# Optimization experiments

Measured on AMD Instinct MI355X. Metric: run time of the kernel, lower is better.

The kernel has to match this reference:

```python
import jax, jax.numpy as jnp
import numpy as np

N = 50000
IN_F = 200
OUT_F = 200
NRELA = 200
E1 = 400000
E2 = 100000
ALPHA = 0.2  # leakyrelu slope


def setup_inputs() -> dict:
    key = jax.random.key(0)
    ks = jax.random.split(key, 9)
    xav = float(np.sqrt(2.0 / (OUT_F + 2 * IN_F + NRELA))) * 1.414
    return {
        "x": jax.random.normal(ks[0], (N, IN_F), dtype=jnp.float32),
        "edge": jax.random.randint(ks[1], (2, E1), 0, N, dtype=jnp.int32),
        "edge_embed": jax.random.normal(ks[2], (E1, NRELA), dtype=jnp.float32),
        "edge_list_nhop": jax.random.randint(ks[3], (2, E2), 0, N, dtype=jnp.int32),
        "edge_embed_nhop": jax.random.normal(ks[4], (E2, NRELA), dtype=jnp.float32),
        "a": jax.random.normal(ks[5], (OUT_F, 2 * IN_F + NRELA), dtype=jnp.float32) * xav,
        "a_2": jax.random.normal(ks[6], (1, OUT_F), dtype=jnp.float32) * float(np.sqrt(2.0 / (1 + OUT_F))) * 1.414,
        "mlp_w": jax.random.normal(ks[7], (1, OUT_F), dtype=jnp.float32) * float(np.sqrt(1.0 / OUT_F)),
        "mlp_b": jnp.zeros((1,), dtype=jnp.float32),
    }


def reference(x, edge, edge_embed, edge_list_nhop, edge_embed_nhop, a, a_2, mlp_w, mlp_b):
    # concat 1-hop and n-hop edges: e [2,E], emb [E,nrela]
    e = jnp.concatenate([edge, edge_list_nhop], axis=1)
    emb = jnp.concatenate([edge_embed, edge_embed_nhop], axis=0)
    src = e[0]
    dst = e[1]
    n_edges = emb.shape[0]
    # edge_h: [E, 2*in + nrela]
    edge_h = jnp.concatenate([x[src], x[dst], emb], axis=1)
    # edge_m = a @ edge_h.T, kept as [E, out]
    edge_m = edge_h @ a.T
    # powers = -leakyrelu(a_2 @ edge_m): [E]
    powers = -jax.nn.leaky_relu(edge_m @ a_2[0], ALPHA)
    # inline MLP: tanh(Linear(edge_m)) -> [E]
    y = jnp.tanh(edge_m @ mlp_w[0] + mlp_b[0])
    powers = powers * y / n_edges
    edge_e = jnp.exp(powers)  # [E]
    n = x.shape[0]
    # segment-sum over source nodes (sparse.sum over dim=1 of coo[src,dst,:])
    e_rowsum = jax.ops.segment_sum(edge_e, src, num_segments=n)[:, None]  # [N,1]
    e_rowsum = jnp.where(e_rowsum == 0.0, 1e-12, e_rowsum)
    # weighted scatter-add of edge messages
    edge_w = edge_e[:, None] * edge_m  # [E, out]
    h_prime = jax.ops.segment_sum(edge_w, src, num_segments=n)  # [N, out]
    h_prime = h_prime / e_rowsum
    return jax.nn.elu(h_prime)  # concat=True
```

## Files before the change

kernel.cpp:

```cpp
#include <hip/hip_runtime.h>
#include <math.h>

#define NN    50000
#define FDIM  200
#define E1N   400000
#define E2N   100000
#define EN    500000

typedef __attribute__((ext_vector_type(8))) short short8;
typedef __attribute__((ext_vector_type(4))) float f32x4;

#define VALL_OFF   0
#define WALL_OFF   608
#define SCAL_OFF   1216
#define RS_OFF     201216
#define CNT_OFF    251216
#define FILL_OFF   301216
#define INCL_OFF   351216
#define BSUM_OFF   401216
#define SORT_OFF   401472
#define XB_OFF     1401472
#define AB_OFF     6401472
#define TSB_OFF    6461472

static __device__ __forceinline__ unsigned short f2bf(float f) {
    unsigned int u = __float_as_uint(f);
    unsigned int r = (u + 0x7fffu + ((u >> 16) & 1u)) >> 16;
    return (unsigned short)r;
}
static __device__ __forceinline__ float bf2f(unsigned short s) {
    return __uint_as_float((unsigned int)s << 16);
}

__global__ void k_coeffs(const float* __restrict__ a, const float* __restrict__ a2,
                         const float* __restrict__ mlpw,
                         float* __restrict__ vall, float* __restrict__ wall) {
    int k = blockIdx.x * blockDim.x + threadIdx.x;
    if (k >= 600) return;
    float v = 0.f, w = 0.f;
    for (int o = 0; o < FDIM; ++o) {
        float av = a[o * 600 + k];
        v += a2[o] * av;
        w += mlpw[o] * av;
    }
    vall[k] = v;
    wall[k] = w;
}

__global__ __launch_bounds__(256) void k_node_scal(const float* __restrict__ x,
                                                   const float* __restrict__ vall,
                                                   const float* __restrict__ wall,
                                                   float* __restrict__ scal,
                                                   unsigned short* __restrict__ xb) {
    __shared__ float sv[1200];
    int tid = threadIdx.x;
    for (int i = tid; i < 1200; i += 256) sv[i] = (i < 600) ? vall[i] : wall[i - 600];
    __syncthreads();
    int lane = tid & 63;
    int n = blockIdx.x * 4 + (tid >> 6);
    float ps = 0.f, pd = 0.f, qs = 0.f, qd = 0.f;
    if (lane < 50) {
        float4 xv = *(const float4*)(x + (size_t)n * FDIM + lane * 4);
        float4 v1 = *(const float4*)(sv + lane * 4);
        float4 v2 = *(const float4*)(sv + 200 + lane * 4);
        float4 w1 = *(const float4*)(sv + 600 + lane * 4);
        float4 w2 = *(const float4*)(sv + 800 + lane * 4);
        ps = xv.x * v1.x + xv.y * v1.y + xv.z * v1.z + xv.w * v1.w;
        pd = xv.x * v2.x + xv.y * v2.y + xv.z * v2.z + xv.w * v2.w;
        qs = xv.x * w1.x + xv.y * w1.y + xv.z * w1.z + xv.w * w1.w;
        qd = xv.x * w2.x + xv.y * w2.y + xv.z * w2.z + xv.w * w2.w;
        ushort4 o;
        o.x = f2bf(xv.x); o.y = f2bf(xv.y); o.z = f2bf(xv.z); o.w = f2bf(xv.w);
        *(ushort4*)(xb + (size_t)n * FDIM + lane * 4) = o;
    }
    #pragma unroll
    for (int off = 32; off > 0; off >>= 1) {
        ps += __shfl_xor(ps, off);
        pd += __shfl_xor(pd, off);
        qs += __shfl_xor(qs, off);
        qd += __shfl_xor(qd, off);
    }
    if (lane == 0) {
        float4 r = make_float4(ps, pd, qs, qd);
        *(float4*)(scal + (size_t)n * 4) = r;
    }
}

__global__ __launch_bounds__(256) void k_cvt(const float* __restrict__ src,
                                             unsigned short* __restrict__ dst, int n4) {
    int i = blockIdx.x * 256 + threadIdx.x;
    if (i >= n4) return;
    float4 v = *(const float4*)(src + (size_t)i * 4);
    ushort4 o;
    o.x = f2bf(v.x); o.y = f2bf(v.y); o.z = f2bf(v.z); o.w = f2bf(v.w);
    *(ushort4*)(dst + (size_t)i * 4) = o;
}

__global__ __launch_bounds__(256) void k_hist(const int* __restrict__ edge,
                                              const int* __restrict__ edgenh,
                                              int* __restrict__ counts) {
    int g = blockIdx.x * 256 + threadIdx.x;
    if (g >= EN) return;
    int s = (g < E1N) ? edge[g] : edgenh[g - E1N];
    atomicAdd(counts + s, 1);
}

__global__ __launch_bounds__(256) void k_scan1(const int* __restrict__ counts,
                                               int* __restrict__ incl,
                                               int* __restrict__ bsums) {
    __shared__ int tmp[256];
    int g = blockIdx.x * 256 + threadIdx.x;
    int v = (g < NN) ? counts[g] : 0;
    tmp[threadIdx.x] = v;
    __syncthreads();
    for (int off = 1; off < 256; off <<= 1) {
        int t = (threadIdx.x >= off) ? tmp[threadIdx.x - off] : 0;
        __syncthreads();
        tmp[threadIdx.x] += t;
        __syncthreads();
    }
    if (g < NN) incl[g] = tmp[threadIdx.x];
    if (threadIdx.x == 255) bsums[blockIdx.x] = tmp[255];
}

__global__ __launch_bounds__(256) void k_scan2(int* __restrict__ bsums, int nb) {
    __shared__ int tmp[256];
    int v = (threadIdx.x < nb) ? bsums[threadIdx.x] : 0;
    tmp[threadIdx.x] = v;
    __syncthreads();
    for (int off = 1; off < 256; off <<= 1) {
        int t = (threadIdx.x >= off) ? tmp[threadIdx.x - off] : 0;
        __syncthreads();
        tmp[threadIdx.x] += t;
        __syncthreads();
    }
    if (threadIdx.x < nb) bsums[threadIdx.x] = tmp[threadIdx.x] - v;
}

__global__ __launch_bounds__(256) void k_scan3(const int* __restrict__ counts,
                                               int* __restrict__ incl,
                                               const int* __restrict__ bsums,
                                               int* __restrict__ fill) {
    int g = blockIdx.x * 256 + threadIdx.x;
    if (g >= NN) return;
    int v = incl[g] - counts[g] + bsums[blockIdx.x];
    incl[g] = v;
    fill[g] = v;
}

__global__ __launch_bounds__(256) void k_scatter(const int* __restrict__ edge,
                                                 const int* __restrict__ edgenh,
                                                 int* __restrict__ fill,
                                                 int2* __restrict__ sorted2) {
    int g = blockIdx.x * 256 + threadIdx.x;
    if (g >= EN) return;
    int s, d;
    if (g < E1N) { s = edge[g]; d = edge[E1N + g]; }
    else { s = edgenh[g - E1N]; d = edgenh[E2N + (g - E1N)]; }
    int pos = atomicAdd(fill + s, 1);
    sorted2[pos] = make_int2(g, d);
}

__global__ __launch_bounds__(256) void k_csr(const int2* __restrict__ sorted2,
                                             const int* __restrict__ offs,
                                             const int* __restrict__ counts,
                                             const float* __restrict__ ee,
                                             const float* __restrict__ eenh,
                                             const unsigned short* __restrict__ xb,
                                             const float* __restrict__ vall,
                                             const float* __restrict__ wall,
                                             const float* __restrict__ scal,
                                             const float* __restrict__ mlpb,
                                             float* __restrict__ rowsum,
                                             unsigned short* __restrict__ Tsb) {
    int tid = threadIdx.x, lane = tid & 63;
    int n = blockIdx.x * 4 + (tid >> 6);
    float4 v3 = make_float4(0, 0, 0, 0), w3 = v3;
    if (lane < 50) {
        v3 = *(const float4*)(vall + 400 + lane * 4);
        w3 = *(const float4*)(wall + 400 + lane * 4);
    }
    float4 sc_n = *(const float4*)(scal + (size_t)n * 4);
    float mb = mlpb[0];
    int beg = offs[n], cnt = counts[n];
    float accx0 = 0, accx1 = 0, accx2 = 0, accx3 = 0;
    float acce0 = 0, acce1 = 0, acce2 = 0, acce3 = 0;
    float rs = 0.f;
    int2 ed = (cnt > 0) ? sorted2[beg] : make_int2(0, 0);
    for (int i = 0; i < cnt; ++i) {
        int2 ed_n = (i + 1 < cnt) ? sorted2[beg + i + 1] : ed;
        int e = ed.x, d = ed.y;
        const float* erow = (e < E1N) ? ee + (size_t)e * FDIM
                                      : eenh + (size_t)(e - E1N) * FDIM;
        float4 ev = make_float4(0, 0, 0, 0), xv = ev;
        if (lane < 50) {
            ev = *(const float4*)(erow + lane * 4);
            ushort4 xu = *(const ushort4*)(xb + (size_t)d * FDIM + lane * 4);
            xv.x = bf2f(xu.x); xv.y = bf2f(xu.y); xv.z = bf2f(xu.z); xv.w = bf2f(xu.w);
        }
        float pe = ev.x * v3.x + ev.y * v3.y + ev.z * v3.z + ev.w * v3.w;
        float qe = ev.x * w3.x + ev.y * w3.y + ev.z * w3.z + ev.w * w3.w;
        #pragma unroll
        for (int off = 32; off > 0; off >>= 1) {
            pe += __shfl_xor(pe, off);
            qe += __shfl_xor(qe, off);
        }
        float4 sd = *(const float4*)(scal + (size_t)d * 4);
        float z1 = sc_n.x + sd.y + pe;
        float z2 = sc_n.z + sd.w + qe + mb;
        float l = z1 > 0.f ? z1 : 0.2f * z1;
        float e2 = __expf(2.f * z2);
        float t = 1.f - 2.f * __builtin_amdgcn_rcpf(e2 + 1.f);
        float wgt = __expf(l * t * (-1.f / (float)EN));
        rs += wgt;
        accx0 += wgt * xv.x; accx1 += wgt * xv.y; accx2 += wgt * xv.z; accx3 += wgt * xv.w;
        acce0 += wgt * ev.x; acce1 += wgt * ev.y; acce2 += wgt * ev.z; acce3 += wgt * ev.w;
        ed = ed_n;
    }
    if (lane == 0) rowsum[n] = rs;
    float inv = (cnt > 0) ? __builtin_amdgcn_rcpf(rs) : 0.f;
    if (lane < 50) {
        ushort4 o1, o2;
        o1.x = f2bf(accx0 * inv); o1.y = f2bf(accx1 * inv);
        o1.z = f2bf(accx2 * inv); o1.w = f2bf(accx3 * inv);
        o2.x = f2bf(acce0 * inv); o2.y = f2bf(acce1 * inv);
        o2.z = f2bf(acce2 * inv); o2.w = f2bf(acce3 * inv);
        *(ushort4*)(Tsb + (size_t)n * 400 + lane * 4) = o1;
        *(ushort4*)(Tsb + (size_t)n * 400 + 200 + lane * 4) = o2;
    }
}

__global__ __launch_bounds__(256) void k_gemm_fused(const unsigned short* __restrict__ xb,
                                                    const unsigned short* __restrict__ tsb,
                                                    const unsigned short* __restrict__ ab,
                                                    const float* __restrict__ rowsum,
                                                    float* __restrict__ out) {
    __shared__ unsigned short Al[64][40];
    __shared__ unsigned short Bl[64][40];
    int tid = threadIdx.x, w = tid >> 6, lane = tid & 63;
    int bx = blockIdx.x, by = blockIdx.y;
    f32x4 acc[4] = {};
    int r = tid >> 2, c = tid & 3;
    int arow = by * 64 + r;
    int brow = bx * 64 + r;
    bool inA = arow < NN;
    bool inB = brow < 200;
    const unsigned short* aPx = xb + (size_t)arow * 200;
    const unsigned short* aPt = tsb + (size_t)arow * 400;
    const unsigned short* bP = ab + (size_t)brow * 600;
    for (int k0 = 0; k0 < 640; k0 += 32) {
        int gk = k0 + c * 8;
        uint4 av = make_uint4(0, 0, 0, 0), bv = av;
        if (gk < 200) {
            if (inA) av = *(const uint4*)(aPx + gk);
            if (inB) bv = *(const uint4*)(bP + gk);
        } else if (gk >= 224 && gk < 624) {
            if (inA) av = *(const uint4*)(aPt + (gk - 224));
            if (inB) bv = *(const uint4*)(bP + gk - 24);
        }
        *(uint4*)&Al[r][c * 8] = av;
        *(uint4*)&Bl[r][c * 8] = bv;
        __syncthreads();
        short8 af = *(short8*)&Al[w * 16 + (lane & 15)][(lane >> 4) * 8];
        #pragma unroll
        for (int ct = 0; ct < 4; ++ct) {
            short8 bf = *(short8*)&Bl[ct * 16 + (lane & 15)][(lane >> 4) * 8];
            acc[ct] = __builtin_amdgcn_mfma_f32_16x16x32_bf16(af, bf, acc[ct], 0, 0, 0);
        }
        __syncthreads();
    }
    #pragma unroll
    for (int ct = 0; ct < 4; ++ct) {
        #pragma unroll
        for (int rr = 0; rr < 4; ++rr) {
            int grow = by * 64 + w * 16 + (lane >> 4) * 4 + rr;
            int gcol = bx * 64 + ct * 16 + (lane & 15);
            if (grow < NN && gcol < 200) {
                float rsv = rowsum[grow];
                float h = acc[ct][rr];
                float o = (rsv == 0.f) ? 0.f : (h > 0.f ? h : expm1f(h));
                out[(size_t)grow * 200 + gcol] = o;
            }
        }
    }
}

extern "C" void kernel_launch(void* const* d_in, const int* in_sizes, int n_in,
                              void* d_out, int out_size, void* d_ws, size_t ws_size,
                              hipStream_t stream) {
    const float* x      = (const float*)d_in[0];
    const int*   edge   = (const int*)d_in[1];
    const float* ee     = (const float*)d_in[2];
    const int*   edgenh = (const int*)d_in[3];
    const float* eenh   = (const float*)d_in[4];
    const float* a      = (const float*)d_in[5];
    const float* a2     = (const float*)d_in[6];
    const float* mlpw   = (const float*)d_in[7];
    const float* mlpb   = (const float*)d_in[8];

    float* ws = (float*)d_ws;
    float* vall   = ws + VALL_OFF;
    float* wall   = ws + WALL_OFF;
    float* scal   = ws + SCAL_OFF;
    float* rowsum = ws + RS_OFF;
    int*   counts = (int*)(ws + CNT_OFF);
    int*   fill   = (int*)(ws + FILL_OFF);
    int*   incl   = (int*)(ws + INCL_OFF);
    int*   bsums  = (int*)(ws + BSUM_OFF);
    int2*  sorted2 = (int2*)(ws + SORT_OFF);
    unsigned short* xb  = (unsigned short*)(ws + XB_OFF);
    unsigned short* ab  = (unsigned short*)(ws + AB_OFF);
    unsigned short* tsb = (unsigned short*)(ws + TSB_OFF);

    hipMemsetAsync(counts, 0, (size_t)(2 * NN) * sizeof(int), stream);

    k_coeffs<<<3, 256, 0, stream>>>(a, a2, mlpw, vall, wall);
    k_node_scal<<<NN / 4, 256, 0, stream>>>(x, vall, wall, scal, xb);
    k_cvt<<<(200 * 600 / 4 + 255) / 256, 256, 0, stream>>>(a, ab, 200 * 600 / 4);

    k_hist<<<(EN + 255) / 256, 256, 0, stream>>>(edge, edgenh, counts);
    int nb = (NN + 255) / 256;
    k_scan1<<<nb, 256, 0, stream>>>(counts, incl, bsums);
    k_scan2<<<1, 256, 0, stream>>>(bsums, nb);
    k_scan3<<<nb, 256, 0, stream>>>(counts, incl, bsums, fill);
    k_scatter<<<(EN + 255) / 256, 256, 0, stream>>>(edge, edgenh, fill, sorted2);

    k_csr<<<NN / 4, 256, 0, stream>>>(sorted2, incl, counts, ee, eenh, xb,
                                      vall, wall, scal, mlpb, rowsum, tsb);

    dim3 gg(4, (NN + 63) / 64);
    k_gemm_fused<<<gg, 256, 0, stream>>>(xb, tsb, ab, rowsum, (float*)d_out);
}
```

Measured before the change: 747.2 us.

## Use DPP wave reductions, prefetch next edge rows, remap GEMM block order

```diff
diff --git a/kernel.cpp b/kernel.cpp
--- a/kernel.cpp
+++ b/kernel.cpp
@@ -30,6 +30,19 @@
 }
 static __device__ __forceinline__ float bf2f(unsigned short s) {
     return __uint_as_float((unsigned int)s << 16);
+}
+
+#define DPP_ADD(x, ctrl, rmask) \
+    x += __int_as_float(__builtin_amdgcn_update_dpp(0, __float_as_int(x), ctrl, rmask, 0xf, true))
+
+static __device__ __forceinline__ float wave_sum_bcast(float x) {
+    DPP_ADD(x, 0x111, 0xf);
+    DPP_ADD(x, 0x112, 0xf);
+    DPP_ADD(x, 0x114, 0xf);
+    DPP_ADD(x, 0x118, 0xf);
+    DPP_ADD(x, 0x142, 0xa);
+    DPP_ADD(x, 0x143, 0xc);
+    return __int_as_float(__builtin_amdgcn_readlane(__float_as_int(x), 63));
 }
 
 __global__ void k_coeffs(const float* __restrict__ a, const float* __restrict__ a2,
@@ -73,13 +86,10 @@
         o.x = f2bf(xv.x); o.y = f2bf(xv.y); o.z = f2bf(xv.z); o.w = f2bf(xv.w);
         *(ushort4*)(xb + (size_t)n * FDIM + lane * 4) = o;
     }
-    #pragma unroll
-    for (int off = 32; off > 0; off >>= 1) {
-        ps += __shfl_xor(ps, off);
-        pd += __shfl_xor(pd, off);
-        qs += __shfl_xor(qs, off);
-        qd += __shfl_xor(qd, off);
-    }
+    ps = wave_sum_bcast(ps);
+    pd = wave_sum_bcast(pd);
+    qs = wave_sum_bcast(qs);
+    qd = wave_sum_bcast(qd);
     if (lane == 0) {
         float4 r = make_float4(ps, pd, qs, qd);
         *(float4*)(scal + (size_t)n * 4) = r;
@@ -187,25 +197,29 @@
     float acce0 = 0, acce1 = 0, acce2 = 0, acce3 = 0;
     float rs = 0.f;
     int2 ed = (cnt > 0) ? sorted2[beg] : make_int2(0, 0);
+    float4 evc = make_float4(0, 0, 0, 0), xvc = evc;
+    if (cnt > 0 && lane < 50) {
+        const float* er = (ed.x < E1N) ? ee + (size_t)ed.x * FDIM
+                                       : eenh + (size_t)(ed.x - E1N) * FDIM;
+        evc = *(const float4*)(er + lane * 4);
+        ushort4 xu = *(const ushort4*)(xb + (size_t)ed.y * FDIM + lane * 4);
+        xvc.x = bf2f(xu.x); xvc.y = bf2f(xu.y); xvc.z = bf2f(xu.z); xvc.w = bf2f(xu.w);
+    }
     for (int i = 0; i < cnt; ++i) {
-        int2 ed_n = (i + 1 < cnt) ? sorted2[beg + i + 1] : ed;
-        int e = ed.x, d = ed.y;
-        const float* erow = (e < E1N) ? ee + (size_t)e * FDIM
-                                      : eenh + (size_t)(e - E1N) * FDIM;
-        float4 ev = make_float4(0, 0, 0, 0), xv = ev;
-        if (lane < 50) {
-            ev = *(const float4*)(erow + lane * 4);
-            ushort4 xu = *(const ushort4*)(xb + (size_t)d * FDIM + lane * 4);
-            xv.x = bf2f(xu.x); xv.y = bf2f(xu.y); xv.z = bf2f(xu.z); xv.w = bf2f(xu.w);
+        int2 edn = (i + 1 < cnt) ? sorted2[beg + i + 1] : ed;
+        float4 evn = make_float4(0, 0, 0, 0), xvn = evn;
+        if (i + 1 < cnt && lane < 50) {
+            const float* ern = (edn.x < E1N) ? ee + (size_t)edn.x * FDIM
+                                             : eenh + (size_t)(edn.x - E1N) * FDIM;
+            evn = *(const float4*)(ern + lane * 4);
+            ushort4 xu = *(const ushort4*)(xb + (size_t)edn.y * FDIM + lane * 4);
+            xvn.x = bf2f(xu.x); xvn.y = bf2f(xu.y); xvn.z = bf2f(xu.z); xvn.w = bf2f(xu.w);
         }
-        float pe = ev.x * v3.x + ev.y * v3.y + ev.z * v3.z + ev.w * v3.w;
-        float qe = ev.x * w3.x + ev.y * w3.y + ev.z * w3.z + ev.w * w3.w;
-        #pragma unroll
-        for (int off = 32; off > 0; off >>= 1) {
-            pe += __shfl_xor(pe, off);
-            qe += __shfl_xor(qe, off);
-        }
-        float4 sd = *(const float4*)(scal + (size_t)d * 4);
+        float pe = evc.x * v3.x + evc.y * v3.y + evc.z * v3.z + evc.w * v3.w;
+        float qe = evc.x * w3.x + evc.y * w3.y + evc.z * w3.z + evc.w * w3.w;
+        pe = wave_sum_bcast(pe);
+        qe = wave_sum_bcast(qe);
+        float4 sd = *(const float4*)(scal + (size_t)ed.y * 4);
         float z1 = sc_n.x + sd.y + pe;
         float z2 = sc_n.z + sd.w + qe + mb;
         float l = z1 > 0.f ? z1 : 0.2f * z1;
@@ -213,9 +227,9 @@
         float t = 1.f - 2.f * __builtin_amdgcn_rcpf(e2 + 1.f);
         float wgt = __expf(l * t * (-1.f / (float)EN));
         rs += wgt;
-        accx0 += wgt * xv.x; accx1 += wgt * xv.y; accx2 += wgt * xv.z; accx3 += wgt * xv.w;
-        acce0 += wgt * ev.x; acce1 += wgt * ev.y; acce2 += wgt * ev.z; acce3 += wgt * ev.w;
-        ed = ed_n;
+        accx0 += wgt * xvc.x; accx1 += wgt * xvc.y; accx2 += wgt * xvc.z; accx3 += wgt * xvc.w;
+        acce0 += wgt * evc.x; acce1 += wgt * evc.y; acce2 += wgt * evc.z; acce3 += wgt * evc.w;
+        ed = edn; evc = evn; xvc = xvn;
     }
     if (lane == 0) rowsum[n] = rs;
     float inv = (cnt > 0) ? __builtin_amdgcn_rcpf(rs) : 0.f;
@@ -238,7 +252,9 @@
     __shared__ unsigned short Al[64][40];
     __shared__ unsigned short Bl[64][40];
     int tid = threadIdx.x, w = tid >> 6, lane = tid & 63;
-    int bx = blockIdx.x, by = blockIdx.y;
+    int h = blockIdx.y * 4 + blockIdx.x;
+    int g = (h & 7) * 391 + (h >> 3);
+    int by = g >> 2, bx = g & 3;
     f32x4 acc[4] = {};
     int r = tid >> 2, c = tid & 3;
     int arow = by * 64 + r;
@@ -277,8 +293,8 @@
             int gcol = bx * 64 + ct * 16 + (lane & 15);
             if (grow < NN && gcol < 200) {
                 float rsv = rowsum[grow];
-                float h = acc[ct][rr];
-                float o = (rsv == 0.f) ? 0.f : (h > 0.f ? h : expm1f(h));
+                float hh = acc[ct][rr];
+                float o = (rsv == 0.f) ? 0.f : (hh > 0.f ? hh : expm1f(hh));
                 out[(size_t)grow * 200 + gcol] = o;
             }
         }
```

Result: faster. 727.6 us (-2.6%).
